# Kernel optimization log

Hardware: AMD Instinct MI355X
Metric: run time of the kernel (lower is better)

## Reference

```python
import jax, jax.numpy as jnp
import numpy as np

N = 20000      # nodes
M = 16         # fixed neighbor fanout
FEAT = 500     # input feature dim
KD = 16        # per-capsule dim (k_dim)
CAPS = [8, 7, 6, 5, 4, 3]  # out_caps per layer (first_channel=8, dec_k=1, nlayer=6)
ROUTIT = 5
TAU = 1.0


def _l2(x, axis):
    # F.normalize with eps=1e-12
    return x / jnp.maximum(jnp.sqrt(jnp.sum(x * x, axis=axis, keepdims=True)), 1e-12)


def _routing(x, nb, k, d):
    # x: [n, k*d], nb: [n*m] int neighbor ids
    n = x.shape[0]
    m = nb.shape[0] // n
    x = _l2(x.reshape(n, k, d), 2)                       # [n,k,d] per-capsule normalize
    z = x.reshape(n, k * d)[nb].reshape(n, m, k, d)      # neighbor gather
    u = x
    for t in range(ROUTIT):
        p = jnp.einsum('nmkd,nkd->nmk', z, u)            # agreement scores
        p = jax.nn.softmax(p / TAU, axis=2)              # softmax over capsules
        u = jnp.einsum('nmkd,nmk->nkd', z, p) + x        # aggregate + self
        if t < ROUTIT - 1:
            u = _l2(u, 2)
    return u.reshape(n, k * d)


def setup_inputs() -> dict:
    key = jax.random.key(0)
    ks = jax.random.split(key, 16)
    inp = {}
    inp['feature'] = jax.random.normal(ks[0], (N, FEAT), dtype=jnp.float32)
    inp['neighbor_id'] = jax.random.randint(ks[1], (N, M), 0, N)
    s = 1.0 / np.sqrt(FEAT)
    inp['pca_w'] = jax.random.uniform(ks[2], (CAPS[0] * KD, FEAT), minval=-s, maxval=s, dtype=jnp.float32)
    inp['pca_b'] = jax.random.uniform(ks[3], (CAPS[0] * KD,), minval=-s, maxval=s, dtype=jnp.float32)
    for i in range(1, len(CAPS)):
        fin, fout = CAPS[i - 1] * KD, CAPS[i] * KD
        s = 1.0 / np.sqrt(fin)
        inp[f'w{i}'] = jax.random.uniform(ks[2 * i + 2], (fout, fin), minval=-s, maxval=s, dtype=jnp.float32)
        inp[f'b{i}'] = jax.random.uniform(ks[2 * i + 3], (fout,), minval=-s, maxval=s, dtype=jnp.float32)
    return inp


def reference(feature, neighbor_id, pca_w, pca_b, w1, b1, w2, b2, w3, b3, w4, b4, w5, b5):
    nb = neighbor_id.reshape(-1)
    lin = [None, (w1, b1), (w2, b2), (w3, b3), (w4, b4), (w5, b5)]
    # SparseInput: dropout(relu(linear(x))) -- dropout is identity in eval mode
    x = jax.nn.relu(feature @ pca_w.T + pca_b)
    xs = [x]
    for i, k in enumerate(CAPS):
        if lin[i] is not None:
            w, b = lin[i]
            x = x @ w.T + b
        x = jax.nn.relu(_routing(x, nb, k, KD))
        xs.append(x)
    return jnp.concatenate(xs, axis=1)  # jump connections -> [N, 656]
```

## Files before the change

kernel.cpp:

```cpp
#include <hip/hip_runtime.h>
#include <hip/hip_bf16.h>
#include <cstdint>
#include <cstddef>

#define NNODES 20000
#define MNB    16
#define NFEAT  500
#define OUTC   656

typedef short short8 __attribute__((ext_vector_type(8)));
typedef float floatx4 __attribute__((ext_vector_type(4)));
typedef float v2f __attribute__((ext_vector_type(2)));

__device__ __forceinline__ float bf2f(unsigned int h) {
    union { unsigned int u; float f; } v; v.u = h << 16; return v.f;
}
__device__ __forceinline__ unsigned short f2bf(float f) {
    union { float f; unsigned int u; } v; v.f = f;
    unsigned int u = v.u;
    u += 0x7FFFu + ((u >> 16) & 1u);
    return (unsigned short)(u >> 16);
}

__device__ __forceinline__ v2f pk_mul(v2f a, v2f b) {
    v2f d;
    asm("v_pk_mul_f32 %0, %1, %2 op_sel:[0,0] op_sel_hi:[1,1]"
        : "=v"(d) : "v"(a), "v"(b));
    return d;
}
__device__ __forceinline__ v2f pk_fma(v2f a, v2f b, v2f c) {
    v2f d;
    asm("v_pk_fma_f32 %0, %1, %2, %3 op_sel:[0,0,0] op_sel_hi:[1,1,1]"
        : "=v"(d) : "v"(a), "v"(b), "v"(c));
    return d;
}
__device__ __forceinline__ v2f pk_add(v2f a, v2f b) {
    v2f d;
    asm("v_pk_add_f32 %0, %1, %2 op_sel:[0,0] op_sel_hi:[1,1]"
        : "=v"(d) : "v"(a), "v"(b));
    return d;
}

#define PIN(x) asm volatile("" : "+v"(x))

template<int CTRL>
__device__ __forceinline__ float dpp_add(float v) {
    const int o = __builtin_amdgcn_update_dpp(0, __float_as_int(v), CTRL, 0xF, 0xF, true);
    return v + __int_as_float(o);
}
__device__ __forceinline__ float sum16(float v) {
    v = dpp_add<0xB1>(v);
    v = dpp_add<0x4E>(v);
    v = dpp_add<0x141>(v);
    v = dpp_add<0x140>(v);
    return v;
}

__global__ __launch_bounds__(64) void detect_kernel(const unsigned short* __restrict__ fx,
                                                    int* __restrict__ flag) {
    const int tid = threadIdx.x;
    const unsigned short s = fx[2 * tid];
    const int e = (s >> 7) & 0xFF;
    const bool ok = (e >= 100 && e <= 140);
    const unsigned long long m = __ballot(ok);
    if (tid == 0) *flag = (__popcll(m) >= 32) ? 1 : 0;
}

struct WPtrs { const void* p[12]; };

__global__ __launch_bounds__(256) void convert_weights(WPtrs ptrs, const int* __restrict__ flag,
                                                       float* __restrict__ outb) {
    constexpr int SN[12] = {64000,128,14336,112,10752,96,7680,80,5120,64,3072,48};
    constexpr int SO[12] = {0,64000,64128,78464,78576,89328,89424,97104,97184,102304,102368,105440};
    constexpr int TOT = 105488;
    const int i = blockIdx.x * 256 + threadIdx.x;
    if (i >= TOT) return;
    const bool isbf = (*flag != 0);
    int seg = 0, local = i;
#pragma unroll
    for (int s = 0; s < 12; ++s) {
        if (i >= SO[s] && i < SO[s] + SN[s]) { seg = s; local = i - SO[s]; }
    }
    const void* src = ptrs.p[seg];
    float v;
    if (isbf) v = bf2f(((const unsigned short*)src)[local]);
    else      v = ((const float*)src)[local];
    outb[i] = v;
}

__global__ __launch_bounds__(256) void convert_wpad(const float* __restrict__ wblob,
                                                    unsigned short* __restrict__ wpad) {
    const int i = blockIdx.x * 256 + threadIdx.x;
    const int n = i >> 9, k = i & 511;
    const float v = (k < NFEAT) ? wblob[n * NFEAT + k] : 0.f;
    wpad[i] = f2bf(v);
}

__global__ __launch_bounds__(256) void pca_mfma(
    const void* __restrict__ feat_raw,
    const unsigned short* __restrict__ wpad,
    const float* __restrict__ bias,
    const int* __restrict__ flag,
    float* __restrict__ xn,
    void* __restrict__ out_raw)
{
    __shared__ short sA[32 * 56];
    __shared__ short sB[128 * 56];
    const int tid = threadIdx.x;
    const int l = tid & 63, wv = tid >> 6;
    const int m = l & 15, q = l >> 4;
    const int rt = wv >> 1, ch = wv & 1;
    const int r0 = blockIdx.x * 32;
    const bool isbf = (*flag != 0);

    const int arow = tid >> 3, aseg = tid & 7;

    floatx4 acc[4];
#pragma unroll
    for (int t = 0; t < 4; ++t) acc[t] = 0;

    for (int c = 0; c < 16; ++c) {
        const int k0 = c * 32;
        __syncthreads();
        {
            const int k = k0 + aseg * 4;
            uint2 v = make_uint2(0u, 0u);
            if (k < NFEAT) {
                if (isbf) {
                    v = *(const uint2*)((const unsigned short*)feat_raw +
                                        (size_t)(r0 + arow) * NFEAT + k);
                } else {
                    const float4 f = *(const float4*)((const float*)feat_raw +
                                                      (size_t)(r0 + arow) * NFEAT + k);
                    v.x = ((unsigned int)f2bf(f.y) << 16) | f2bf(f.x);
                    v.y = ((unsigned int)f2bf(f.w) << 16) | f2bf(f.z);
                }
            }
            *(uint2*)&sA[arow * 56 + aseg * 4] = v;
        }
#pragma unroll
        for (int it = 0; it < 4; ++it) {
            const int idx = tid + 256 * it;
            const int row = idx >> 3, seg = idx & 7;
            const uint2 v = *(const uint2*)(wpad + (size_t)row * 512 + k0 + seg * 4);
            *(uint2*)&sB[row * 56 + seg * 4] = v;
        }
        __syncthreads();
        const short8 af = *(const short8*)&sA[(rt * 16 + m) * 56 + q * 8];
#pragma unroll
        for (int t = 0; t < 4; ++t) {
            const short8 bf = *(const short8*)&sB[((ch * 4 + t) * 16 + m) * 56 + q * 8];
            acc[t] = __builtin_amdgcn_mfma_f32_16x16x32_bf16(af, bf, acc[t], 0, 0, 0);
        }
    }

#pragma unroll
    for (int t = 0; t < 4; ++t) {
        const int col = (ch * 4 + t) * 16 + m;
        const float bb = bias[col];
#pragma unroll
        for (int r = 0; r < 4; ++r) {
            const int grow = r0 + rt * 16 + q * 4 + r;
            const float y = fmaxf(acc[t][r] + bb, 0.f);
            if (isbf) ((unsigned short*)out_raw)[(size_t)grow * OUTC + col] = f2bf(y);
            else      ((float*)out_raw)[(size_t)grow * OUTC + col] = y;
            const float ss = sum16(y * y);
            const float invn = 1.0f / fmaxf(sqrtf(ss), 1e-12f);
            xn[(size_t)grow * 128 + col] = y * invn;
        }
    }
}

template<int FIN, int FOUT>
__global__ __launch_bounds__(256) void linear_mfma(
    const float* __restrict__ xin,
    const float* __restrict__ w,
    const float* __restrict__ bias,
    float* __restrict__ xn)
{
    constexpr int KP   = ((FIN + 31) / 32) * 32;
    constexpr int NCH  = KP / 32;
    constexpr int NTIL = 2 * (FOUT / 16);
    constexpr int MT   = (NTIL + 3) / 4;
    __shared__ short sAh[32 * 56], sAl[32 * 56];
    __shared__ short sBh[FOUT * 56], sBl[FOUT * 56];
    const int tid = threadIdx.x;
    const int l = tid & 63, wv = tid >> 6;
    const int m = l & 15, q = l >> 4;
    const int n0 = blockIdx.x * 32;

    floatx4 acc[MT];
#pragma unroll
    for (int i = 0; i < MT; ++i) acc[i] = 0;

    for (int c = 0; c < NCH; ++c) {
        const int k0 = c * 32;
        __syncthreads();
        {
            const int row = tid >> 3, seg = tid & 7;
            const int k = k0 + seg * 4;
            uint2 vh = make_uint2(0u, 0u), vl = make_uint2(0u, 0u);
            if (k < FIN) {
                const float4 f = *(const float4*)(xin + (size_t)(n0 + row) * FIN + k);
                const unsigned short h0 = f2bf(f.x), h1 = f2bf(f.y);
                const unsigned short h2 = f2bf(f.z), h3 = f2bf(f.w);
                const unsigned short e0 = f2bf(f.x - bf2f(h0)), e1 = f2bf(f.y - bf2f(h1));
                const unsigned short e2 = f2bf(f.z - bf2f(h2)), e3 = f2bf(f.w - bf2f(h3));
                vh = make_uint2(((unsigned)h1 << 16) | h0, ((unsigned)h3 << 16) | h2);
                vl = make_uint2(((unsigned)e1 << 16) | e0, ((unsigned)e3 << 16) | e2);
            }
            *(uint2*)&sAh[row * 56 + seg * 4] = vh;
            *(uint2*)&sAl[row * 56 + seg * 4] = vl;
        }
        for (int idx = tid; idx < FOUT * 8; idx += 256) {
            const int row = idx >> 3, seg = idx & 7;
            const int k = k0 + seg * 4;
            uint2 vh = make_uint2(0u, 0u), vl = make_uint2(0u, 0u);
            if (k < FIN) {
                const float4 f = *(const float4*)(w + (size_t)row * FIN + k);
                const unsigned short h0 = f2bf(f.x), h1 = f2bf(f.y);
                const unsigned short h2 = f2bf(f.z), h3 = f2bf(f.w);
                const unsigned short e0 = f2bf(f.x - bf2f(h0)), e1 = f2bf(f.y - bf2f(h1));
                const unsigned short e2 = f2bf(f.z - bf2f(h2)), e3 = f2bf(f.w - bf2f(h3));
                vh = make_uint2(((unsigned)h1 << 16) | h0, ((unsigned)h3 << 16) | h2);
                vl = make_uint2(((unsigned)e1 << 16) | e0, ((unsigned)e3 << 16) | e2);
            }
            *(uint2*)&sBh[row * 56 + seg * 4] = vh;
            *(uint2*)&sBl[row * 56 + seg * 4] = vl;
        }
        __syncthreads();
#pragma unroll
        for (int ti = 0; ti < MT; ++ti) {
            const int t = wv + ti * 4;
            if (t < NTIL) {
                const int rt = t & 1, ct = t >> 1;
                const int ao = (rt * 16 + m) * 56 + q * 8;
                const int bo = (ct * 16 + m) * 56 + q * 8;
                const short8 ah = *(const short8*)&sAh[ao];
                const short8 al = *(const short8*)&sAl[ao];
                const short8 bh = *(const short8*)&sBh[bo];
                const short8 bl = *(const short8*)&sBl[bo];
                floatx4 a = acc[ti];
                a = __builtin_amdgcn_mfma_f32_16x16x32_bf16(ah, bh, a, 0, 0, 0);
                a = __builtin_amdgcn_mfma_f32_16x16x32_bf16(ah, bl, a, 0, 0, 0);
                a = __builtin_amdgcn_mfma_f32_16x16x32_bf16(al, bh, a, 0, 0, 0);
                acc[ti] = a;
            }
        }
    }
#pragma unroll
    for (int ti = 0; ti < MT; ++ti) {
        const int t = wv + ti * 4;
        if (t < NTIL) {
            const int rt = t & 1, ct = t >> 1;
            const int col = ct * 16 + m;
            const float bb = bias[col];
#pragma unroll
            for (int r = 0; r < 4; ++r) {
                const int grow = n0 + rt * 16 + q * 4 + r;
                const float y = acc[ti][r] + bb;
                const float ss = sum16(y * y);
                const float invn = __builtin_amdgcn_rsqf(fmaxf(ss, 1e-24f));
                xn[(size_t)grow * FOUT + col] = y * invn;
            }
        }
    }
}

template<int K, int NPW>
__global__ __launch_bounds__(256, 1) void routing_v11(
    const float* __restrict__ xn,
    const int* __restrict__ nb,
    float* __restrict__ xout,
    void* __restrict__ out_raw,
    const int* __restrict__ flag,
    const int coloff)
{
    constexpr int KD16 = K * 16;
    const int tid = threadIdx.x;
    const int l = tid & 63, wv = tid >> 6;
    const int m = l & 7;
    const int k = (l >> 3) & (NPW == 2 ? 3 : 7);
    const int nsub = (NPW == 2) ? (l >> 5) : 0;
    const int node = blockIdx.x * (4 * NPW) + wv * NPW + nsub;
    const bool kv = (k < K);
    const bool isbf = (*flag != 0);
    const int nid0 = nb[(size_t)node * 16 + m];
    const int nid1 = nb[(size_t)node * 16 + m + 8];

    v2f z0[8], z1[8], x[8], u[8];
    {
        const float* z0p = xn + (size_t)nid0 * KD16 + k * 16;
        const float* z1p = xn + (size_t)nid1 * KD16 + k * 16;
        const float* xp  = xn + (size_t)node * KD16 + k * 16;
#pragma unroll
        for (int q = 0; q < 4; ++q) {
            float4 a = make_float4(0.f, 0.f, 0.f, 0.f);
            float4 b = a, c = a;
            if (kv) {
                a = *(const float4*)(z0p + q * 4);
                b = *(const float4*)(z1p + q * 4);
                c = *(const float4*)(xp  + q * 4);
            }
            z0[2 * q] = (v2f){a.x, a.y}; z0[2 * q + 1] = (v2f){a.z, a.w};
            z1[2 * q] = (v2f){b.x, b.y}; z1[2 * q + 1] = (v2f){b.z, b.w};
            x[2 * q]  = (v2f){c.x, c.y}; x[2 * q + 1]  = (v2f){c.z, c.w};
            u[2 * q]  = (v2f){c.x, c.y}; u[2 * q + 1]  = (v2f){c.z, c.w};
        }
    }
#pragma unroll
    for (int h = 0; h < 8; ++h) { PIN(z0[h]); PIN(z1[h]); PIN(x[h]); }
    float invn = 1.0f;

    for (int t = 0; t < 5; ++t) {
        v2f d0 = pk_mul(z0[0], u[0]);
        v2f d1 = pk_mul(z1[0], u[0]);
#pragma unroll
        for (int h = 1; h < 8; ++h) {
            d0 = pk_fma(z0[h], u[h], d0);
            d1 = pk_fma(z1[h], u[h], d1);
        }
        const float p0 = kv ? (d0[0] + d0[1]) * invn : -1e4f;
        const float p1 = kv ? (d1[0] + d1[1]) * invn : -1e4f;
        float e0 = __expf(p0), e1 = __expf(p1);
        float s0 = dpp_add<0x128>(e0);
        float s1 = dpp_add<0x128>(e1);
        s0 += __shfl_xor(s0, 16);
        s1 += __shfl_xor(s1, 16);
        if (NPW == 1) {
            s0 += __shfl_xor(s0, 32);
            s1 += __shfl_xor(s1, 32);
        }
        e0 *= __builtin_amdgcn_rcpf(s0);
        e1 *= __builtin_amdgcn_rcpf(s1);
        const v2f ev0 = {e0, e0}, ev1 = {e1, e1};
#pragma unroll
        for (int h = 0; h < 8; ++h)
            u[h] = pk_fma(ev1, z1[h], pk_mul(ev0, z0[h]));
#pragma unroll
        for (int h = 0; h < 8; ++h) { u[h][0] = dpp_add<0xB1>(u[h][0]);  u[h][1] = dpp_add<0xB1>(u[h][1]); }
#pragma unroll
        for (int h = 0; h < 8; ++h) { u[h][0] = dpp_add<0x4E>(u[h][0]);  u[h][1] = dpp_add<0x4E>(u[h][1]); }
#pragma unroll
        for (int h = 0; h < 8; ++h) { u[h][0] = dpp_add<0x141>(u[h][0]); u[h][1] = dpp_add<0x141>(u[h][1]); }
#pragma unroll
        for (int h = 0; h < 8; ++h) u[h] = pk_add(u[h], x[h]);
        if (t < 4) {
            v2f n0 = pk_mul(u[0], u[0]);
            v2f n1 = pk_mul(u[1], u[1]);
#pragma unroll
            for (int h = 2; h < 8; h += 2) {
                n0 = pk_fma(u[h],     u[h],     n0);
                n1 = pk_fma(u[h + 1], u[h + 1], n1);
            }
            invn = __builtin_amdgcn_rsqf(fmaxf(n0[0] + n0[1] + n1[0] + n1[1], 1e-24f));
        }
    }

#pragma unroll
    for (int h = 0; h < 8; ++h) {
        u[h][0] = fmaxf(u[h][0], 0.f);
        u[h][1] = fmaxf(u[h][1], 0.f);
    }
    if (kv && m < 4) {
        v2f a = u[0], b = u[1];
        if (m == 1)      { a = u[2]; b = u[3]; }
        else if (m == 2) { a = u[4]; b = u[5]; }
        else if (m == 3) { a = u[6]; b = u[7]; }
        const float4 w4 = make_float4(a[0], a[1], b[0], b[1]);
        *(float4*)(xout + (size_t)node * KD16 + k * 16 + m * 4) = w4;
        const size_t ooff = (size_t)node * OUTC + coloff + k * 16 + m * 4;
        if (isbf) {
            uint2 pk;
            pk.x = ((unsigned int)f2bf(w4.y) << 16) | f2bf(w4.x);
            pk.y = ((unsigned int)f2bf(w4.w) << 16) | f2bf(w4.z);
            *(uint2*)((unsigned short*)out_raw + ooff) = pk;
        } else {
            *(float4*)((float*)out_raw + ooff) = w4;
        }
    }
}

extern "C" void kernel_launch(void* const* d_in, const int* in_sizes, int n_in,
                              void* d_out, int out_size, void* d_ws, size_t ws_size,
                              hipStream_t stream) {
    const int* nbid = (const int*)d_in[1];

    int*            flag  = (int*)d_ws;
    float*          wblob = (float*)((char*)d_ws + 16);
    unsigned short* wpad  = (unsigned short*)((char*)d_ws + (448 << 10));
    float*          xn    = (float*)((char*)d_ws + (1 << 20));
    float*          xc    = xn + (size_t)NNODES * 128;

    float* pw = wblob +      0; float* pb = wblob +  64000;
    float* w1 = wblob +  64128; float* b1 = wblob +  78464;
    float* w2 = wblob +  78576; float* b2 = wblob +  89328;
    float* w3 = wblob +  89424; float* b3 = wblob +  97104;
    float* w4 = wblob +  97184; float* b4 = wblob + 102304;
    float* w5 = wblob + 102368; float* b5 = wblob + 105440;

    hipLaunchKernelGGL(detect_kernel, dim3(1), dim3(64), 0, stream,
                       (const unsigned short*)d_in[0], flag);

    WPtrs wp;
    for (int i = 0; i < 12; ++i) wp.p[i] = d_in[i + 2];
    hipLaunchKernelGGL(convert_weights, dim3(413), dim3(256), 0, stream, wp, flag, wblob);
    hipLaunchKernelGGL(convert_wpad, dim3(256), dim3(256), 0, stream, pw, wpad);

    hipLaunchKernelGGL(pca_mfma, dim3(NNODES / 32), dim3(256), 0, stream,
                       d_in[0], wpad, pb, flag, xn, d_out);

    const int g1 = NNODES / 4;
    const int g2 = NNODES / 8;
    const int lgrid = NNODES / 32;

    hipLaunchKernelGGL((routing_v11<8, 1>), dim3(g1), dim3(256), 0, stream,
                       xn, nbid, xc, d_out, flag, 128);
    hipLaunchKernelGGL((linear_mfma<128, 112>), dim3(lgrid), dim3(256), 0, stream,
                       xc, w1, b1, xn);

    hipLaunchKernelGGL((routing_v11<7, 1>), dim3(g1), dim3(256), 0, stream,
                       xn, nbid, xc, d_out, flag, 256);
    hipLaunchKernelGGL((linear_mfma<112, 96>), dim3(lgrid), dim3(256), 0, stream,
                       xc, w2, b2, xn);

    hipLaunchKernelGGL((routing_v11<6, 1>), dim3(g1), dim3(256), 0, stream,
                       xn, nbid, xc, d_out, flag, 368);
    hipLaunchKernelGGL((linear_mfma<96, 80>), dim3(lgrid), dim3(256), 0, stream,
                       xc, w3, b3, xn);

    hipLaunchKernelGGL((routing_v11<5, 1>), dim3(g1), dim3(256), 0, stream,
                       xn, nbid, xc, d_out, flag, 464);
    hipLaunchKernelGGL((linear_mfma<80, 64>), dim3(lgrid), dim3(256), 0, stream,
                       xc, w4, b4, xn);

    hipLaunchKernelGGL((routing_v11<4, 2>), dim3(g2), dim3(256), 0, stream,
                       xn, nbid, xc, d_out, flag, 544);
    hipLaunchKernelGGL((linear_mfma<64, 48>), dim3(lgrid), dim3(256), 0, stream,
                       xc, w5, b5, xn);

    hipLaunchKernelGGL((routing_v11<3, 2>), dim3(g2), dim3(256), 0, stream,
                       xn, nbid, xc, d_out, flag, 608);
}
```

Measured before the change: 373.7 us.

## Fuse routing with following linear layer using transposed fp32 weights

Each routing layer now feeds its ReLU output through shared memory straight into the next layer's linear, bias and per-capsule normalize, all in one kernel. This replaces the separate bf16x3 MFMA linear kernels. It removes a global round trip of the intermediate activations and five kernel launches, and adds a one-time weight transpose kernel. In exchange the GEMM now runs as scalar fp32 FMAs reading weights from global/L2 per node, and launch_bounds(256,1) may limit occupancy.

Result: slower. 512.4 us (+37.1%).

```diff
diff --git a/kernel.cpp b/kernel.cpp
--- a/kernel.cpp
+++ b/kernel.cpp
@@ -86,6 +86,24 @@
     if (isbf) v = bf2f(((const unsigned short*)src)[local]);
     else      v = ((const float*)src)[local];
     outb[i] = v;
+}
+
+__global__ __launch_bounds__(256) void convert_wt(const float* __restrict__ wblob,
+                                                  float* __restrict__ wt) {
+    constexpr int NF[5]   = {128, 112, 96, 80, 64};
+    constexpr int NO[5]   = {112, 96, 80, 64, 48};
+    constexpr int WOFF[5] = {64128, 78576, 89424, 97184, 102368};
+    constexpr int TOFF[5] = {0, 14336, 25088, 32768, 37888};
+    constexpr int TOT = 40960;
+    const int i = blockIdx.x * 256 + threadIdx.x;
+    if (i >= TOT) return;
+    int s = 0;
+#pragma unroll
+    for (int t = 1; t < 5; ++t) if (i >= TOFF[t]) s = t;
+    const int local = i - TOFF[s];
+    const int r = local / NO[s];
+    const int c = local % NO[s];
+    wt[i] = wblob[WOFF[s] + c * NF[s] + r];
 }
 
 __global__ __launch_bounds__(256) void convert_wpad(const float* __restrict__ wblob,
@@ -167,102 +185,6 @@
             const float ss = sum16(y * y);
             const float invn = 1.0f / fmaxf(sqrtf(ss), 1e-12f);
             xn[(size_t)grow * 128 + col] = y * invn;
-        }
-    }
-}
-
-template<int FIN, int FOUT>
-__global__ __launch_bounds__(256) void linear_mfma(
-    const float* __restrict__ xin,
-    const float* __restrict__ w,
-    const float* __restrict__ bias,
-    float* __restrict__ xn)
-{
-    constexpr int KP   = ((FIN + 31) / 32) * 32;
-    constexpr int NCH  = KP / 32;
-    constexpr int NTIL = 2 * (FOUT / 16);
-    constexpr int MT   = (NTIL + 3) / 4;
-    __shared__ short sAh[32 * 56], sAl[32 * 56];
-    __shared__ short sBh[FOUT * 56], sBl[FOUT * 56];
-    const int tid = threadIdx.x;
-    const int l = tid & 63, wv = tid >> 6;
-    const int m = l & 15, q = l >> 4;
-    const int n0 = blockIdx.x * 32;
-
-    floatx4 acc[MT];
-#pragma unroll
-    for (int i = 0; i < MT; ++i) acc[i] = 0;
-
-    for (int c = 0; c < NCH; ++c) {
-        const int k0 = c * 32;
-        __syncthreads();
-        {
-            const int row = tid >> 3, seg = tid & 7;
-            const int k = k0 + seg * 4;
-            uint2 vh = make_uint2(0u, 0u), vl = make_uint2(0u, 0u);
-            if (k < FIN) {
-                const float4 f = *(const float4*)(xin + (size_t)(n0 + row) * FIN + k);
-                const unsigned short h0 = f2bf(f.x), h1 = f2bf(f.y);
-                const unsigned short h2 = f2bf(f.z), h3 = f2bf(f.w);
-                const unsigned short e0 = f2bf(f.x - bf2f(h0)), e1 = f2bf(f.y - bf2f(h1));
-                const unsigned short e2 = f2bf(f.z - bf2f(h2)), e3 = f2bf(f.w - bf2f(h3));
-                vh = make_uint2(((unsigned)h1 << 16) | h0, ((unsigned)h3 << 16) | h2);
-                vl = make_uint2(((unsigned)e1 << 16) | e0, ((unsigned)e3 << 16) | e2);
-            }
-            *(uint2*)&sAh[row * 56 + seg * 4] = vh;
-            *(uint2*)&sAl[row * 56 + seg * 4] = vl;
-        }
-        for (int idx = tid; idx < FOUT * 8; idx += 256) {
-            const int row = idx >> 3, seg = idx & 7;
-            const int k = k0 + seg * 4;
-            uint2 vh = make_uint2(0u, 0u), vl = make_uint2(0u, 0u);
-            if (k < FIN) {
-                const float4 f = *(const float4*)(w + (size_t)row * FIN + k);
-                const unsigned short h0 = f2bf(f.x), h1 = f2bf(f.y);
-                const unsigned short h2 = f2bf(f.z), h3 = f2bf(f.w);
-                const unsigned short e0 = f2bf(f.x - bf2f(h0)), e1 = f2bf(f.y - bf2f(h1));
-                const unsigned short e2 = f2bf(f.z - bf2f(h2)), e3 = f2bf(f.w - bf2f(h3));
-                vh = make_uint2(((unsigned)h1 << 16) | h0, ((unsigned)h3 << 16) | h2);
-                vl = make_uint2(((unsigned)e1 << 16) | e0, ((unsigned)e3 << 16) | e2);
-            }
-            *(uint2*)&sBh[row * 56 + seg * 4] = vh;
-            *(uint2*)&sBl[row * 56 + seg * 4] = vl;
-        }
-        __syncthreads();
-#pragma unroll
-        for (int ti = 0; ti < MT; ++ti) {
-            const int t = wv + ti * 4;
-            if (t < NTIL) {
-                const int rt = t & 1, ct = t >> 1;
-                const int ao = (rt * 16 + m) * 56 + q * 8;
-                const int bo = (ct * 16 + m) * 56 + q * 8;
-                const short8 ah = *(const short8*)&sAh[ao];
-                const short8 al = *(const short8*)&sAl[ao];
-                const short8 bh = *(const short8*)&sBh[bo];
-                const short8 bl = *(const short8*)&sBl[bo];
-                floatx4 a = acc[ti];
-                a = __builtin_amdgcn_mfma_f32_16x16x32_bf16(ah, bh, a, 0, 0, 0);
-                a = __builtin_amdgcn_mfma_f32_16x16x32_bf16(ah, bl, a, 0, 0, 0);
-                a = __builtin_amdgcn_mfma_f32_16x16x32_bf16(al, bh, a, 0, 0, 0);
-                acc[ti] = a;
-            }
-        }
-    }
-#pragma unroll
-    for (int ti = 0; ti < MT; ++ti) {
-        const int t = wv + ti * 4;
-        if (t < NTIL) {
-            const int rt = t & 1, ct = t >> 1;
-            const int col = ct * 16 + m;
-            const float bb = bias[col];
-#pragma unroll
-            for (int r = 0; r < 4; ++r) {
-                const int grow = n0 + rt * 16 + q * 4 + r;
-                const float y = acc[ti][r] + bb;
-                const float ss = sum16(y * y);
-                const float invn = __builtin_amdgcn_rsqf(fmaxf(ss, 1e-24f));
-                xn[(size_t)grow * FOUT + col] = y * invn;
-            }
         }
     }
 }
@@ -381,23 +303,181 @@
     }
 }
 
+template<int K, int FOUT, int NPW>
+__global__ __launch_bounds__(256, 1) void routing_linear(
+    const float* __restrict__ xin,
+    float* __restrict__ xnext,
+    const float* __restrict__ wt,
+    const float* __restrict__ bias,
+    const int* __restrict__ nb,
+    void* __restrict__ out_raw,
+    const int* __restrict__ flag,
+    const int coloff)
+{
+    constexpr int KD16 = K * 16;
+    __shared__ float xs[4 * NPW][KD16];
+    const int tid = threadIdx.x;
+    const int l = tid & 63, wv = tid >> 6;
+    const int m = l & 7;
+    const int k = (l >> 3) & (NPW == 2 ? 3 : 7);
+    const int nsub = (NPW == 2) ? (l >> 5) : 0;
+    const int node = blockIdx.x * (4 * NPW) + wv * NPW + nsub;
+    const bool kv = (k < K);
+    const bool isbf = (*flag != 0);
+    const int nid0 = nb[(size_t)node * 16 + m];
+    const int nid1 = nb[(size_t)node * 16 + m + 8];
+
+    v2f z0[8], z1[8], x[8], u[8];
+    {
+        const float* z0p = xin + (size_t)nid0 * KD16 + k * 16;
+        const float* z1p = xin + (size_t)nid1 * KD16 + k * 16;
+        const float* xp  = xin + (size_t)node * KD16 + k * 16;
+#pragma unroll
+        for (int q = 0; q < 4; ++q) {
+            float4 a = make_float4(0.f, 0.f, 0.f, 0.f);
+            float4 b = a, c = a;
+            if (kv) {
+                a = *(const float4*)(z0p + q * 4);
+                b = *(const float4*)(z1p + q * 4);
+                c = *(const float4*)(xp  + q * 4);
+            }
+            z0[2 * q] = (v2f){a.x, a.y}; z0[2 * q + 1] = (v2f){a.z, a.w};
+            z1[2 * q] = (v2f){b.x, b.y}; z1[2 * q + 1] = (v2f){b.z, b.w};
+            x[2 * q]  = (v2f){c.x, c.y}; x[2 * q + 1]  = (v2f){c.z, c.w};
+            u[2 * q]  = (v2f){c.x, c.y}; u[2 * q + 1]  = (v2f){c.z, c.w};
+        }
+    }
+#pragma unroll
+    for (int h = 0; h < 8; ++h) { PIN(z0[h]); PIN(z1[h]); PIN(x[h]); }
+    float invn = 1.0f;
+
+    for (int t = 0; t < 5; ++t) {
+        v2f d0 = pk_mul(z0[0], u[0]);
+        v2f d1 = pk_mul(z1[0], u[0]);
+#pragma unroll
+        for (int h = 1; h < 8; ++h) {
+            d0 = pk_fma(z0[h], u[h], d0);
+            d1 = pk_fma(z1[h], u[h], d1);
+        }
+        const float p0 = kv ? (d0[0] + d0[1]) * invn : -1e4f;
+        const float p1 = kv ? (d1[0] + d1[1]) * invn : -1e4f;
+        float e0 = __expf(p0), e1 = __expf(p1);
+        float s0 = dpp_add<0x128>(e0);
+        float s1 = dpp_add<0x128>(e1);
+        s0 += __shfl_xor(s0, 16);
+        s1 += __shfl_xor(s1, 16);
+        if (NPW == 1) {
+            s0 += __shfl_xor(s0, 32);
+            s1 += __shfl_xor(s1, 32);
+        }
+        e0 *= __builtin_amdgcn_rcpf(s0);
+        e1 *= __builtin_amdgcn_rcpf(s1);
+        const v2f ev0 = {e0, e0}, ev1 = {e1, e1};
+#pragma unroll
+        for (int h = 0; h < 8; ++h)
+            u[h] = pk_fma(ev1, z1[h], pk_mul(ev0, z0[h]));
+#pragma unroll
+        for (int h = 0; h < 8; ++h) { u[h][0] = dpp_add<0xB1>(u[h][0]);  u[h][1] = dpp_add<0xB1>(u[h][1]); }
+#pragma unroll
+        for (int h = 0; h < 8; ++h) { u[h][0] = dpp_add<0x4E>(u[h][0]);  u[h][1] = dpp_add<0x4E>(u[h][1]); }
+#pragma unroll
+        for (int h = 0; h < 8; ++h) { u[h][0] = dpp_add<0x141>(u[h][0]); u[h][1] = dpp_add<0x141>(u[h][1]); }
+#pragma unroll
+        for (int h = 0; h < 8; ++h) u[h] = pk_add(u[h], x[h]);
+        if (t < 4) {
+            v2f n0 = pk_mul(u[0], u[0]);
+            v2f n1 = pk_mul(u[1], u[1]);
+#pragma unroll
+            for (int h = 2; h < 8; h += 2) {
+                n0 = pk_fma(u[h],     u[h],     n0);
+                n1 = pk_fma(u[h + 1], u[h + 1], n1);
+            }
+            invn = __builtin_amdgcn_rsqf(fmaxf(n0[0] + n0[1] + n1[0] + n1[1], 1e-24f));
+        }
+    }
+
+#pragma unroll
+    for (int h = 0; h < 8; ++h) {
+        u[h][0] = fmaxf(u[h][0], 0.f);
+        u[h][1] = fmaxf(u[h][1], 0.f);
+    }
+    if (kv && m < 4) {
+        v2f a = u[0], b = u[1];
+        if (m == 1)      { a = u[2]; b = u[3]; }
+        else if (m == 2) { a = u[4]; b = u[5]; }
+        else if (m == 3) { a = u[6]; b = u[7]; }
+        const float4 w4 = make_float4(a[0], a[1], b[0], b[1]);
+        *(float4*)&xs[wv * NPW + nsub][k * 16 + m * 4] = w4;
+        const size_t ooff = (size_t)node * OUTC + coloff + k * 16 + m * 4;
+        if (isbf) {
+            uint2 pk;
+            pk.x = ((unsigned int)f2bf(w4.y) << 16) | f2bf(w4.x);
+            pk.y = ((unsigned int)f2bf(w4.w) << 16) | f2bf(w4.z);
+            *(uint2*)((unsigned short*)out_raw + ooff) = pk;
+        } else {
+            *(float4*)((float*)out_raw + ooff) = w4;
+        }
+    }
+    __syncthreads();
+
+    constexpr int FIN = KD16;
+    const int lo2  = (NPW == 1) ? l : (l & 31);
+    const int nidx = (NPW == 1) ? wv : (wv * 2 + (l >> 5));
+    const int node2 = blockIdx.x * (4 * NPW) + nidx;
+    const bool act = (2 * lo2 < FOUT);
+    const int oo = act ? 2 * lo2 : 0;
+    v2f acc = {0.f, 0.f};
+    const float* wrow = wt + oo;
+#pragma unroll 4
+    for (int i = 0; i < FIN; i += 4) {
+        const float4 xq = *(const float4*)&xs[nidx][i];
+        const v2f w0 = *(const v2f*)(wrow + (size_t)(i + 0) * FOUT);
+        const v2f w1 = *(const v2f*)(wrow + (size_t)(i + 1) * FOUT);
+        const v2f w2 = *(const v2f*)(wrow + (size_t)(i + 2) * FOUT);
+        const v2f w3 = *(const v2f*)(wrow + (size_t)(i + 3) * FOUT);
+        acc = pk_fma(w0, (v2f){xq.x, xq.x}, acc);
+        acc = pk_fma(w1, (v2f){xq.y, xq.y}, acc);
+        acc = pk_fma(w2, (v2f){xq.z, xq.z}, acc);
+        acc = pk_fma(w3, (v2f){xq.w, xq.w}, acc);
+    }
+    {
+        const float2 bb = *(const float2*)(bias + oo);
+        acc = pk_add(acc, (v2f){bb.x, bb.y});
+        float ssp = acc[0] * acc[0] + acc[1] * acc[1];
+        ssp = dpp_add<0xB1>(ssp);
+        ssp = dpp_add<0x4E>(ssp);
+        ssp = dpp_add<0x141>(ssp);
+        const float invq = __builtin_amdgcn_rsqf(fmaxf(ssp, 1e-24f));
+        acc = pk_mul(acc, (v2f){invq, invq});
+        if (act) *(float2*)(xnext + (size_t)node2 * FOUT + oo) = make_float2(acc[0], acc[1]);
+    }
+}
+
 extern "C" void kernel_launch(void* const* d_in, const int* in_sizes, int n_in,
                               void* d_out, int out_size, void* d_ws, size_t ws_size,
                               hipStream_t stream) {
     const int* nbid = (const int*)d_in[1];
 
-    int*            flag  = (int*)d_ws;
-    float*          wblob = (float*)((char*)d_ws + 16);
-    unsigned short* wpad  = (unsigned short*)((char*)d_ws + (448 << 10));
-    float*          xn    = (float*)((char*)d_ws + (1 << 20));
-    float*          xc    = xn + (size_t)NNODES * 128;
-
-    float* pw = wblob +      0; float* pb = wblob +  64000;
-    float* w1 = wblob +  64128; float* b1 = wblob +  78464;
-    float* w2 = wblob +  78576; float* b2 = wblob +  89328;
-    float* w3 = wblob +  89424; float* b3 = wblob +  97104;
-    float* w4 = wblob +  97184; float* b4 = wblob + 102304;
-    float* w5 = wblob + 102368; float* b5 = wblob + 105440;
+    int*            flag   = (int*)d_ws;
+    float*          wblob  = (float*)((char*)d_ws + 16);
+    unsigned short* wpad   = (unsigned short*)((char*)d_ws + (448 << 10));
+    float*          wtblob = (float*)((char*)d_ws + (640 << 10));
+    float*          xnA    = (float*)((char*)d_ws + (1 << 20));
+    float*          xnB    = xnA + (size_t)NNODES * 128;
+
+    float* pb = wblob +  64000;
+    float* b1 = wblob +  78464;
+    float* b2 = wblob +  89328;
+    float* b3 = wblob +  97104;
+    float* b4 = wblob + 102304;
+    float* b5 = wblob + 105440;
+    float* pw = wblob;
+
+    float* wt1 = wtblob +     0;
+    float* wt2 = wtblob + 14336;
+    float* wt3 = wtblob + 25088;
+    float* wt4 = wtblob + 32768;
+    float* wt5 = wtblob + 37888;
 
     hipLaunchKernelGGL(detect_kernel, dim3(1), dim3(64), 0, stream,
                        (const unsigned short*)d_in[0], flag);
@@ -406,39 +486,24 @@
     for (int i = 0; i < 12; ++i) wp.p[i] = d_in[i + 2];
     hipLaunchKernelGGL(convert_weights, dim3(413), dim3(256), 0, stream, wp, flag, wblob);
     hipLaunchKernelGGL(convert_wpad, dim3(256), dim3(256), 0, stream, pw, wpad);
+    hipLaunchKernelGGL(convert_wt, dim3(160), dim3(256), 0, stream, wblob, wtblob);
 
     hipLaunchKernelGGL(pca_mfma, dim3(NNODES / 32), dim3(256), 0, stream,
-                       d_in[0], wpad, pb, flag, xn, d_out);
+                       d_in[0], wpad, pb, flag, xnA, d_out);
 
     const int g1 = NNODES / 4;
     const int g2 = NNODES / 8;
-    const int lgrid = NNODES / 32;
-
-    hipLaunchKernelGGL((routing_v11<8, 1>), dim3(g1), dim3(256), 0, stream,
-                       xn, nbid, xc, d_out, flag, 128);
-    hipLaunchKernelGGL((linear_mfma<128, 112>), dim3(lgrid), dim3(256), 0, stream,
-                       xc, w1, b1, xn);
-
-    hipLaunchKernelGGL((routing_v11<7, 1>), dim3(g1), dim3(256), 0, stream,
-                       xn, nbid, xc, d_out, flag, 256);
-    hipLaunchKernelGGL((linear_mfma<112, 96>), dim3(lgrid), dim3(256), 0, stream,
-                       xc, w2, b2, xn);
-
-    hipLaunchKernelGGL((routing_v11<6, 1>), dim3(g1), dim3(256), 0, stream,
-                       xn, nbid, xc, d_out, flag, 368);
-    hipLaunchKernelGGL((linear_mfma<96, 80>), dim3(lgrid), dim3(256), 0, stream,
-                       xc, w3, b3, xn);
-
-    hipLaunchKernelGGL((routing_v11<5, 1>), dim3(g1), dim3(256), 0, stream,
-                       xn, nbid, xc, d_out, flag, 464);
-    hipLaunchKernelGGL((linear_mfma<80, 64>), dim3(lgrid), dim3(256), 0, stream,
-                       xc, w4, b4, xn);
-
-    hipLaunchKernelGGL((routing_v11<4, 2>), dim3(g2), dim3(256), 0, stream,
-                       xn, nbid, xc, d_out, flag, 544);
-    hipLaunchKernelGGL((linear_mfma<64, 48>), dim3(lgrid), dim3(256), 0, stream,
-                       xc, w5, b5, xn);
-
+
+    hipLaunchKernelGGL((routing_linear<8, 112, 1>), dim3(g1), dim3(256), 0, stream,
+                       xnA, xnB, wt1, b1, nbid, d_out, flag, 128);
+    hipLaunchKernelGGL((routing_linear<7, 96, 1>), dim3(g1), dim3(256), 0, stream,
+                       xnB, xnA, wt2, b2, nbid, d_out, flag, 256);
+    hipLaunchKernelGGL((routing_linear<6, 80, 1>), dim3(g1), dim3(256), 0, stream,
+                       xnA, xnB, wt3, b3, nbid, d_out, flag, 368);
+    hipLaunchKernelGGL((routing_linear<5, 64, 1>), dim3(g1), dim3(256), 0, stream,
+                       xnB, xnA, wt4, b4, nbid, d_out, flag, 464);
+    hipLaunchKernelGGL((routing_linear<4, 48, 2>), dim3(g2), dim3(256), 0, stream,
+                       xnA, xnB, wt5, b5, nbid, d_out, flag, 544);
     hipLaunchKernelGGL((routing_v11<3, 2>), dim3(g2), dim3(256), 0, stream,
-                       xn, nbid, xc, d_out, flag, 608);
-}
+                       xnB, nbid, xnA, d_out, flag, 608);
+}
```

## Replace split-bf16 MFMA linear layers with fp32 VALU packed-FMA kernel

Applied to the files above, without the earlier changes.

Swaps the small inter-layer linear kernels from a 3-pass bf16-split MFMA GEMM to a plain fp32 VALU kernel using packed FMAs, with weights pre-transposed once by a new convert_wt kernel. Each block handles 8 nodes staged in LDS, and each half-wave computes one node's outputs, four columns per lane, streaming weights from global/L2. The aim is to drop the bf16 hi/lo splitting and MFMA tile overhead for these tiny GEMMs, which also gives exact fp32 accumulation. The cost is more per-lane FMA work and repeated weight reads from cache for every node.

After: 482.7 us. +29.2%, slower.

```diff
diff --git a/kernel.cpp b/kernel.cpp
--- a/kernel.cpp
+++ b/kernel.cpp
@@ -86,6 +86,24 @@
     if (isbf) v = bf2f(((const unsigned short*)src)[local]);
     else      v = ((const float*)src)[local];
     outb[i] = v;
+}
+
+__global__ __launch_bounds__(256) void convert_wt(const float* __restrict__ wblob,
+                                                  float* __restrict__ wt) {
+    constexpr int NF[5]   = {128, 112, 96, 80, 64};
+    constexpr int NO[5]   = {112, 96, 80, 64, 48};
+    constexpr int WOFF[5] = {64128, 78576, 89424, 97184, 102368};
+    constexpr int TOFF[5] = {0, 14336, 25088, 32768, 37888};
+    constexpr int TOT = 40960;
+    const int i = blockIdx.x * 256 + threadIdx.x;
+    if (i >= TOT) return;
+    int s = 0;
+#pragma unroll
+    for (int t = 1; t < 5; ++t) if (i >= TOFF[t]) s = t;
+    const int local = i - TOFF[s];
+    const int r = local / NO[s];
+    const int c = local % NO[s];
+    wt[i] = wblob[WOFF[s] + c * NF[s] + r];
 }
 
 __global__ __launch_bounds__(256) void convert_wpad(const float* __restrict__ wblob,
@@ -172,98 +190,56 @@
 }
 
 template<int FIN, int FOUT>
-__global__ __launch_bounds__(256) void linear_mfma(
+__global__ __launch_bounds__(256) void linear_valu(
     const float* __restrict__ xin,
-    const float* __restrict__ w,
+    const float* __restrict__ wt,
     const float* __restrict__ bias,
     float* __restrict__ xn)
 {
-    constexpr int KP   = ((FIN + 31) / 32) * 32;
-    constexpr int NCH  = KP / 32;
-    constexpr int NTIL = 2 * (FOUT / 16);
-    constexpr int MT   = (NTIL + 3) / 4;
-    __shared__ short sAh[32 * 56], sAl[32 * 56];
-    __shared__ short sBh[FOUT * 56], sBl[FOUT * 56];
+    __shared__ float xs[8][FIN];
     const int tid = threadIdx.x;
+    const int n0 = blockIdx.x * 8;
+    constexpr int NV = 8 * FIN / 4;
+    for (int i = tid; i < NV; i += 256) {
+        *(float4*)&xs[0][i * 4] = *(const float4*)(xin + (size_t)n0 * FIN + i * 4);
+    }
+    __syncthreads();
     const int l = tid & 63, wv = tid >> 6;
-    const int m = l & 15, q = l >> 4;
-    const int n0 = blockIdx.x * 32;
-
-    floatx4 acc[MT];
-#pragma unroll
-    for (int i = 0; i < MT; ++i) acc[i] = 0;
-
-    for (int c = 0; c < NCH; ++c) {
-        const int k0 = c * 32;
-        __syncthreads();
-        {
-            const int row = tid >> 3, seg = tid & 7;
-            const int k = k0 + seg * 4;
-            uint2 vh = make_uint2(0u, 0u), vl = make_uint2(0u, 0u);
-            if (k < FIN) {
-                const float4 f = *(const float4*)(xin + (size_t)(n0 + row) * FIN + k);
-                const unsigned short h0 = f2bf(f.x), h1 = f2bf(f.y);
-                const unsigned short h2 = f2bf(f.z), h3 = f2bf(f.w);
-                const unsigned short e0 = f2bf(f.x - bf2f(h0)), e1 = f2bf(f.y - bf2f(h1));
-                const unsigned short e2 = f2bf(f.z - bf2f(h2)), e3 = f2bf(f.w - bf2f(h3));
-                vh = make_uint2(((unsigned)h1 << 16) | h0, ((unsigned)h3 << 16) | h2);
-                vl = make_uint2(((unsigned)e1 << 16) | e0, ((unsigned)e3 << 16) | e2);
-            }
-            *(uint2*)&sAh[row * 56 + seg * 4] = vh;
-            *(uint2*)&sAl[row * 56 + seg * 4] = vl;
-        }
-        for (int idx = tid; idx < FOUT * 8; idx += 256) {
-            const int row = idx >> 3, seg = idx & 7;
-            const int k = k0 + seg * 4;
-            uint2 vh = make_uint2(0u, 0u), vl = make_uint2(0u, 0u);
-            if (k < FIN) {
-                const float4 f = *(const float4*)(w + (size_t)row * FIN + k);
-                const unsigned short h0 = f2bf(f.x), h1 = f2bf(f.y);
-                const unsigned short h2 = f2bf(f.z), h3 = f2bf(f.w);
-                const unsigned short e0 = f2bf(f.x - bf2f(h0)), e1 = f2bf(f.y - bf2f(h1));
-                const unsigned short e2 = f2bf(f.z - bf2f(h2)), e3 = f2bf(f.w - bf2f(h3));
-                vh = make_uint2(((unsigned)h1 << 16) | h0, ((unsigned)h3 << 16) | h2);
-                vl = make_uint2(((unsigned)e1 << 16) | e0, ((unsigned)e3 << 16) | e2);
-            }
-            *(uint2*)&sBh[row * 56 + seg * 4] = vh;
-            *(uint2*)&sBl[row * 56 + seg * 4] = vl;
-        }
-        __syncthreads();
-#pragma unroll
-        for (int ti = 0; ti < MT; ++ti) {
-            const int t = wv + ti * 4;
-            if (t < NTIL) {
-                const int rt = t & 1, ct = t >> 1;
-                const int ao = (rt * 16 + m) * 56 + q * 8;
-                const int bo = (ct * 16 + m) * 56 + q * 8;
-                const short8 ah = *(const short8*)&sAh[ao];
-                const short8 al = *(const short8*)&sAl[ao];
-                const short8 bh = *(const short8*)&sBh[bo];
-                const short8 bl = *(const short8*)&sBl[bo];
-                floatx4 a = acc[ti];
-                a = __builtin_amdgcn_mfma_f32_16x16x32_bf16(ah, bh, a, 0, 0, 0);
-                a = __builtin_amdgcn_mfma_f32_16x16x32_bf16(ah, bl, a, 0, 0, 0);
-                a = __builtin_amdgcn_mfma_f32_16x16x32_bf16(al, bh, a, 0, 0, 0);
-                acc[ti] = a;
-            }
-        }
-    }
-#pragma unroll
-    for (int ti = 0; ti < MT; ++ti) {
-        const int t = wv + ti * 4;
-        if (t < NTIL) {
-            const int rt = t & 1, ct = t >> 1;
-            const int col = ct * 16 + m;
-            const float bb = bias[col];
-#pragma unroll
-            for (int r = 0; r < 4; ++r) {
-                const int grow = n0 + rt * 16 + q * 4 + r;
-                const float y = acc[ti][r] + bb;
-                const float ss = sum16(y * y);
-                const float invn = __builtin_amdgcn_rsqf(fmaxf(ss, 1e-24f));
-                xn[(size_t)grow * FOUT + col] = y * invn;
-            }
-        }
+    const int nib = wv * 2 + (l >> 5);
+    const int lo = l & 31;
+    const int oo = 4 * lo;
+    const bool act = (oo < FOUT);
+    v2f a0 = {0.f, 0.f}, a1 = {0.f, 0.f}, b0 = {0.f, 0.f}, b1 = {0.f, 0.f};
+    if (act) {
+        const float* wp = wt + oo;
+#pragma unroll 4
+        for (int i = 0; i < FIN; i += 2) {
+            const float4 w0 = *(const float4*)(wp + (size_t)i * FOUT);
+            const float4 w1 = *(const float4*)(wp + (size_t)(i + 1) * FOUT);
+            const float xa = xs[nib][i], xb = xs[nib][i + 1];
+            const v2f va = {xa, xa}, vb = {xb, xb};
+            a0 = pk_fma((v2f){w0.x, w0.y}, va, a0);
+            a1 = pk_fma((v2f){w0.z, w0.w}, va, a1);
+            b0 = pk_fma((v2f){w1.x, w1.y}, vb, b0);
+            b1 = pk_fma((v2f){w1.z, w1.w}, vb, b1);
+        }
+    }
+    v2f y0 = pk_add(a0, b0), y1 = pk_add(a1, b1);
+    if (act) {
+        const float4 bb = *(const float4*)(bias + oo);
+        y0 = pk_add(y0, (v2f){bb.x, bb.y});
+        y1 = pk_add(y1, (v2f){bb.z, bb.w});
+    }
+    float ss = y0[0] * y0[0] + y0[1] * y0[1] + y1[0] * y1[0] + y1[1] * y1[1];
+    if (!act) ss = 0.f;
+    ss = dpp_add<0xB1>(ss);
+    ss = dpp_add<0x4E>(ss);
+    const float invn = __builtin_amdgcn_rsqf(fmaxf(ss, 1e-24f));
+    y0 = pk_mul(y0, (v2f){invn, invn});
+    y1 = pk_mul(y1, (v2f){invn, invn});
+    if (act) {
+        *(float4*)(xn + (size_t)(n0 + nib) * FOUT + oo) =
+            make_float4(y0[0], y0[1], y1[0], y1[1]);
     }
 }
 
@@ -386,18 +362,26 @@
                               hipStream_t stream) {
     const int* nbid = (const int*)d_in[1];
 
-    int*            flag  = (int*)d_ws;
-    float*          wblob = (float*)((char*)d_ws + 16);
-    unsigned short* wpad  = (unsigned short*)((char*)d_ws + (448 << 10));
-    float*          xn    = (float*)((char*)d_ws + (1 << 20));
-    float*          xc    = xn + (size_t)NNODES * 128;
-
-    float* pw = wblob +      0; float* pb = wblob +  64000;
-    float* w1 = wblob +  64128; float* b1 = wblob +  78464;
-    float* w2 = wblob +  78576; float* b2 = wblob +  89328;
-    float* w3 = wblob +  89424; float* b3 = wblob +  97104;
-    float* w4 = wblob +  97184; float* b4 = wblob + 102304;
-    float* w5 = wblob + 102368; float* b5 = wblob + 105440;
+    int*            flag   = (int*)d_ws;
+    float*          wblob  = (float*)((char*)d_ws + 16);
+    unsigned short* wpad   = (unsigned short*)((char*)d_ws + (448 << 10));
+    float*          wtblob = (float*)((char*)d_ws + (640 << 10));
+    float*          xn     = (float*)((char*)d_ws + (1 << 20));
+    float*          xc     = xn + (size_t)NNODES * 128;
+
+    float* pb = wblob +  64000;
+    float* b1 = wblob +  78464;
+    float* b2 = wblob +  89328;
+    float* b3 = wblob +  97104;
+    float* b4 = wblob + 102304;
+    float* b5 = wblob + 105440;
+    float* pw = wblob;
+
+    float* wt1 = wtblob +     0;
+    float* wt2 = wtblob + 14336;
+    float* wt3 = wtblob + 25088;
+    float* wt4 = wtblob + 32768;
+    float* wt5 = wtblob + 37888;
 
     hipLaunchKernelGGL(detect_kernel, dim3(1), dim3(64), 0, stream,
                        (const unsigned short*)d_in[0], flag);
@@ -406,38 +390,39 @@
     for (int i = 0; i < 12; ++i) wp.p[i] = d_in[i + 2];
     hipLaunchKernelGGL(convert_weights, dim3(413), dim3(256), 0, stream, wp, flag, wblob);
     hipLaunchKernelGGL(convert_wpad, dim3(256), dim3(256), 0, stream, pw, wpad);
+    hipLaunchKernelGGL(convert_wt, dim3(160), dim3(256), 0, stream, wblob, wtblob);
 
     hipLaunchKernelGGL(pca_mfma, dim3(NNODES / 32), dim3(256), 0, stream,
                        d_in[0], wpad, pb, flag, xn, d_out);
 
     const int g1 = NNODES / 4;
     const int g2 = NNODES / 8;
-    const int lgrid = NNODES / 32;
+    const int lg = NNODES / 8;
 
     hipLaunchKernelGGL((routing_v11<8, 1>), dim3(g1), dim3(256), 0, stream,
                        xn, nbid, xc, d_out, flag, 128);
-    hipLaunchKernelGGL((linear_mfma<128, 112>), dim3(lgrid), dim3(256), 0, stream,
-                       xc, w1, b1, xn);
+    hipLaunchKernelGGL((linear_valu<128, 112>), dim3(lg), dim3(256), 0, stream,
+                       xc, wt1, b1, xn);
 
     hipLaunchKernelGGL((routing_v11<7, 1>), dim3(g1), dim3(256), 0, stream,
                        xn, nbid, xc, d_out, flag, 256);
-    hipLaunchKernelGGL((linear_mfma<112, 96>), dim3(lgrid), dim3(256), 0, stream,
-                       xc, w2, b2, xn);
+    hipLaunchKernelGGL((linear_valu<112, 96>), dim3(lg), dim3(256), 0, stream,
+                       xc, wt2, b2, xn);
 
     hipLaunchKernelGGL((routing_v11<6, 1>), dim3(g1), dim3(256), 0, stream,
                        xn, nbid, xc, d_out, flag, 368);
-    hipLaunchKernelGGL((linear_mfma<96, 80>), dim3(lgrid), dim3(256), 0, stream,
-                       xc, w3, b3, xn);
+    hipLaunchKernelGGL((linear_valu<96, 80>), dim3(lg), dim3(256), 0, stream,
+                       xc, wt3, b3, xn);
 
     hipLaunchKernelGGL((routing_v11<5, 1>), dim3(g1), dim3(256), 0, stream,
                        xn, nbid, xc, d_out, flag, 464);
-    hipLaunchKernelGGL((linear_mfma<80, 64>), dim3(lgrid), dim3(256), 0, stream,
-                       xc, w4, b4, xn);
+    hipLaunchKernelGGL((linear_valu<80, 64>), dim3(lg), dim3(256), 0, stream,
+                       xc, wt4, b4, xn);
 
     hipLaunchKernelGGL((routing_v11<4, 2>), dim3(g2), dim3(256), 0, stream,
                        xn, nbid, xc, d_out, flag, 544);
-    hipLaunchKernelGGL((linear_mfma<64, 48>), dim3(lgrid), dim3(256), 0, stream,
-                       xc, w5, b5, xn);
+    hipLaunchKernelGGL((linear_valu<64, 48>), dim3(lg), dim3(256), 0, stream,
+                       xc, wt5, b5, xn);
 
     hipLaunchKernelGGL((routing_v11<3, 2>), dim3(g2), dim3(256), 0, stream,
                        xn, nbid, xc, d_out, flag, 608);
```
